# Optimization experiments

Hardware: AMD Instinct MI355X
Metric: run time of the kernel (lower is better)

## Reference

```python
import jax, jax.numpy as jnp
import numpy as np

N_WIRES = 8
DIM = 1 << N_WIRES  # 256

# Precompute CNOT permutations (torchquantum convention: wire 0 = MSB)
_idx = np.arange(DIM)
_CNOT_PERMS = []
for _c in range(N_WIRES):
    _t = (_c + 1) % N_WIRES
    _cbit = (_idx >> (N_WIRES - 1 - _c)) & 1
    _CNOT_PERMS.append(np.where(_cbit == 1, _idx ^ (1 << (N_WIRES - 1 - _t)), _idx))
# PauliZ signs per wire: [DIM, N_WIRES]
_ZSIGNS = np.stack([1.0 - 2.0 * ((_idx >> (N_WIRES - 1 - w)) & 1) for w in range(N_WIRES)], axis=1).astype(np.float32)


def _quantum_heads(x, theta):
    """x: [B,S,H,8] angles; theta: [8]. Returns PauliZ expectations [B,S,H,8].

    Simulates per (token,head) an 8-qubit circuit: RX(x_i+theta_i) on wire i
    (encoder RX followed by trainable RX on same wire = one RX with summed angle),
    then CNOT ring 0->1..6->7, 7->0, then MeasureAll PauliZ.
    """
    B, S, H, _ = x.shape
    N = B * S * H
    ang = x.reshape(N, N_WIRES) + theta  # [N,8]
    state = jnp.zeros((N, DIM), dtype=jnp.complex64).at[:, 0].set(1.0)
    half = ang * 0.5
    c_all = jnp.cos(half)
    s_all = jnp.sin(half)
    for w in range(N_WIRES):
        A = 1 << w
        Bdim = 1 << (N_WIRES - 1 - w)
        s = state.reshape(N, A, 2, Bdim)
        a0, a1 = s[:, :, 0, :], s[:, :, 1, :]
        c = c_all[:, w][:, None, None].astype(jnp.complex64)
        isn = (1j * s_all[:, w][:, None, None]).astype(jnp.complex64)
        n0 = c * a0 - isn * a1
        n1 = -isn * a0 + c * a1
        state = jnp.stack([n0, n1], axis=2).reshape(N, DIM)
    for perm in _CNOT_PERMS:
        state = state[:, perm]
    probs = state.real ** 2 + state.imag ** 2  # [N,256]
    exp = probs @ jnp.asarray(_ZSIGNS)  # [N,8]
    return exp.reshape(B, S, H, N_WIRES)


def _mha(proj, W_combine, num_heads):
    # proj: [B,S,E]; q = k = v = proj (identical deterministic projections)
    B, S, E = proj.shape
    d_k = E // num_heads
    qkv = proj.reshape(B, S, num_heads, d_k).transpose(0, 2, 1, 3)  # [B,H,S,dk]
    scores = jnp.einsum('bhqd,bhkd->bhqk', qkv, qkv) / jnp.sqrt(jnp.float32(d_k))
    attn = jax.nn.softmax(scores, axis=-1)
    out = jnp.einsum('bhqk,bhkd->bhqd', attn, qkv)
    out = out.transpose(0, 2, 1, 3).reshape(B, S, E)
    return out @ W_combine.T


def setup_inputs() -> dict:
    key = jax.random.key(0)
    k1, k2, k3 = jax.random.split(key, 3)
    B, S, H = 8, 1024, 8
    E = H * N_WIRES  # 64
    x = jax.random.normal(k1, (B, S, E), dtype=jnp.float32)
    theta = jax.random.normal(k2, (N_WIRES,), dtype=jnp.float32)
    W_combine = jax.random.normal(k3, (E, E), dtype=jnp.float32) * (1.0 / np.sqrt(E))
    return {'x': x, 'theta': theta, 'W_combine': W_combine}


def reference(x, theta, W_combine):
    B, S, E = x.shape
    H = E // N_WIRES
    proj = _quantum_heads(x.reshape(B, S, H, N_WIRES), theta).reshape(B, S, E)
    return _mha(proj, W_combine, H)
```

## Files before the change

### kernel.cpp

```cpp
#include <hip/hip_runtime.h>

typedef _Float16 half4v __attribute__((ext_vector_type(4)));
typedef __fp16 fp16x2 __attribute__((ext_vector_type(2)));
typedef float float4v __attribute__((ext_vector_type(4)));

#define S_ 1024
#define H_ 8
#define B_ 8
#define BH 64
#define NROW 8192
#define E_ 64
#define VST 1032

static __device__ inline half4v pack4(float a, float b, float c, float d) {
    union { fp16x2 f2[2]; half4v h4; } u;
    u.f2[0] = __builtin_amdgcn_cvt_pkrtz(a, b);
    u.f2[1] = __builtin_amdgcn_cvt_pkrtz(c, d);
    return u.h4;
}

static __device__ inline half4v pack4rne(float a, float b, float c, float d) {
    half4v r = {(_Float16)a, (_Float16)b, (_Float16)c, (_Float16)d};
    return r;
}

__global__ __launch_bounds__(256, 4) void attn_kernel(
        const float* __restrict__ x, const float* __restrict__ theta,
        _Float16* __restrict__ attnH) {
    __shared__ _Float16 kF[64 * 128];
    __shared__ _Float16 vT[9 * VST];
    int bh = blockIdx.x;
    int b = bh >> 3, h = bh & 7;
    int tid = threadIdx.x;

    float th[8];
#pragma unroll
    for (int i = 0; i < 8; ++i) th[i] = theta[i];

    {
        const half4v one = {(_Float16)1.f, (_Float16)1.f, (_Float16)1.f, (_Float16)1.f};
        *(half4v*)&vT[8 * VST + tid * 4] = one;
    }

    for (int s = tid; s < S_; s += 256) {
        const float4* xp = (const float4*)(x + (((size_t)(b << 10) + s) << 6) + (h << 3));
        float4 x0 = xp[0];
        float4 x1 = xp[1];
        float c0 = __cosf(x0.x + th[0]);
        float c1 = __cosf(x0.y + th[1]);
        float c2 = __cosf(x0.z + th[2]);
        float c3 = __cosf(x0.w + th[3]);
        float c4 = __cosf(x1.x + th[4]);
        float c5 = __cosf(x1.y + th[5]);
        float c6 = __cosf(x1.z + th[6]);
        float c7 = __cosf(x1.w + th[7]);
        float e1 = c0 * c1;
        float e2 = e1 * c2;
        float e3 = e2 * c3;
        float e4 = e3 * c4;
        float e5 = e4 * c5;
        float e6 = e5 * c6;
        float e7 = e6 * c7;
        float e0 = ((c1 * c2) * (c3 * c4)) * ((c5 * c6) * c7);
        half4v lo = pack4(e0, e1, e2, e3);
        half4v hi = pack4(e4, e5, e6, e7);
        int kt = s >> 4, c = s & 15;
        *(half4v*)&kF[kt * 128 + c * 4]      = lo;
        *(half4v*)&kF[kt * 128 + 64 + c * 4] = hi;
        vT[0 * VST + s] = lo[0]; vT[1 * VST + s] = lo[1];
        vT[2 * VST + s] = lo[2]; vT[3 * VST + s] = lo[3];
        vT[4 * VST + s] = hi[0]; vT[5 * VST + s] = hi[1];
        vT[6 * VST + s] = hi[2]; vT[7 * VST + s] = hi[3];
    }
    __syncthreads();

    int lane = tid & 63;
    int wv   = tid >> 6;
    int col  = lane & 15;
    int quad = lane >> 4;
    int q0   = blockIdx.y * 64 + wv * 16;

    bool lo2 = (quad < 2);

    int kbase = (lane & 31) * 4;
    int vcol = (col < 9) ? col : (col - 8);
    int vbase = vcol * VST + quad * 4;

    half4v qf = {(_Float16)0.f, (_Float16)0.f, (_Float16)0.f, (_Float16)0.f};
    if (lo2) qf = *(const half4v*)&kF[kbase + (q0 >> 4) * 128];
    qf *= (_Float16)0.51012921f;

    const float4v zc = {0.f, 0.f, 0.f, 0.f};
    float4v o0 = zc, o1 = zc, o2 = zc, o3 = zc;

#pragma unroll
    for (int kt = 0; kt < 16; ++kt) {
        half4v k0 = *(const half4v*)&kF[kbase + (kt +  0) * 128];
        half4v k1 = *(const half4v*)&kF[kbase + (kt + 16) * 128];
        half4v k2 = *(const half4v*)&kF[kbase + (kt + 32) * 128];
        half4v k3 = *(const half4v*)&kF[kbase + (kt + 48) * 128];
        half4v v0 = *(const half4v*)&vT[vbase + (kt +  0) * 16];
        half4v v1 = *(const half4v*)&vT[vbase + (kt + 16) * 16];
        half4v v2 = *(const half4v*)&vT[vbase + (kt + 32) * 16];
        half4v v3 = *(const half4v*)&vT[vbase + (kt + 48) * 16];
        float4v s0 = __builtin_amdgcn_mfma_f32_16x16x16f16(k0, qf, zc, 0, 0, 0);
        float4v s1 = __builtin_amdgcn_mfma_f32_16x16x16f16(k1, qf, zc, 0, 0, 0);
        float4v s2 = __builtin_amdgcn_mfma_f32_16x16x16f16(k2, qf, zc, 0, 0, 0);
        float4v s3 = __builtin_amdgcn_mfma_f32_16x16x16f16(k3, qf, zc, 0, 0, 0);
        half4v p0 = pack4(__builtin_amdgcn_exp2f(s0[0]), __builtin_amdgcn_exp2f(s0[1]),
                          __builtin_amdgcn_exp2f(s0[2]), __builtin_amdgcn_exp2f(s0[3]));
        half4v p1 = pack4(__builtin_amdgcn_exp2f(s1[0]), __builtin_amdgcn_exp2f(s1[1]),
                          __builtin_amdgcn_exp2f(s1[2]), __builtin_amdgcn_exp2f(s1[3]));
        half4v p2 = pack4(__builtin_amdgcn_exp2f(s2[0]), __builtin_amdgcn_exp2f(s2[1]),
                          __builtin_amdgcn_exp2f(s2[2]), __builtin_amdgcn_exp2f(s2[3]));
        half4v p3 = pack4(__builtin_amdgcn_exp2f(s3[0]), __builtin_amdgcn_exp2f(s3[1]),
                          __builtin_amdgcn_exp2f(s3[2]), __builtin_amdgcn_exp2f(s3[3]));
        o0 = __builtin_amdgcn_mfma_f32_16x16x16f16(v0, p0, o0, 0, 0, 0);
        o1 = __builtin_amdgcn_mfma_f32_16x16x16f16(v1, p1, o1, 0, 0, 0);
        o2 = __builtin_amdgcn_mfma_f32_16x16x16f16(v2, p2, o2, 0, 0, 0);
        o3 = __builtin_amdgcn_mfma_f32_16x16x16f16(v3, p3, o3, 0, 0, 0);
    }

    float4v oacc;
#pragma unroll
    for (int r = 0; r < 4; ++r) oacc[r] = (o0[r] + o1[r]) + (o2[r] + o3[r]);

    float l = __shfl(oacc[0], 32 | col, 64);
    if (lo2) {
        float inv = __builtin_amdgcn_rcpf(l);
        half4v ov = pack4(oacc[0] * inv, oacc[1] * inv, oacc[2] * inv, oacc[3] * inv);
        *(half4v*)(attnH + (((size_t)(b << 10) + q0 + col) << 6) + (h << 3) + quad * 4) = ov;
    }
}

__global__ __launch_bounds__(64) void combine_kernel(
        const _Float16* __restrict__ AH, const float* __restrict__ W,
        float* __restrict__ out) {
    int r0 = blockIdx.x * 16;
    int lane = threadIdx.x;
    int col = lane & 15;
    int quad = lane >> 4;

    half4v af[4];
#pragma unroll
    for (int t = 0; t < 4; ++t)
        af[t] = *(const half4v*)&AH[(size_t)(r0 + col) * 64 + t * 16 + quad * 4];

    float4v acc[4] = {{0,0,0,0},{0,0,0,0},{0,0,0,0},{0,0,0,0}};
#pragma unroll
    for (int e = 0; e < 4; ++e) {
#pragma unroll
        for (int t = 0; t < 4; ++t) {
            float4 w4 = *(const float4*)&W[(size_t)(e * 16 + col) * 64 + t * 16 + quad * 4];
            half4v wf = pack4rne(w4.x, w4.y, w4.z, w4.w);
            acc[e] = __builtin_amdgcn_mfma_f32_16x16x16f16(af[t], wf, acc[e], 0, 0, 0);
        }
    }

#pragma unroll
    for (int e = 0; e < 4; ++e)
#pragma unroll
        for (int r = 0; r < 4; ++r)
            out[(size_t)(r0 + quad * 4 + r) * E_ + e * 16 + col] = acc[e][r];
}

extern "C" void kernel_launch(void* const* d_in, const int* in_sizes, int n_in,
                              void* d_out, int out_size, void* d_ws, size_t ws_size,
                              hipStream_t stream) {
    const float* x     = (const float*)d_in[0];
    const float* theta = (const float*)d_in[1];
    const float* W     = (const float*)d_in[2];
    float* out = (float*)d_out;

    _Float16* attnH = (_Float16*)d_ws;

    attn_kernel<<<dim3(BH, S_ / 64), 256, 0, stream>>>(x, theta, attnH);
    combine_kernel<<<NROW / 16, 64, 0, stream>>>(attnH, W, out);
}
```

Measured before the change: 72.44 us.

## Split quantum projection into separate kernel and stage K/V from global

The per-head quantum expectation computation, previously redone by each of the 16 query-tile blocks per (b,h), moves into a dedicated proj_kernel that writes fp16 K and transposed V layouts to workspace once. The attention kernel then bulk-copies these precomputed tiles into LDS with 16-byte loads. This removes 16x redundant cosine and product work per head, at the cost of an extra kernel launch and a global round-trip for K/V. The RNE weight pack helper is also inlined.

```diff
diff --git a/kernel.cpp b/kernel.cpp
--- a/kernel.cpp
+++ b/kernel.cpp
@@ -11,6 +11,8 @@
 #define NROW 8192
 #define E_ 64
 #define VST 1032
+#define VHALVES (9 * VST)
+#define VCHUNK (VHALVES / 8)
 
 static __device__ inline half4v pack4(float a, float b, float c, float d) {
     union { fp16x2 f2[2]; half4v h4; } u;
@@ -19,58 +21,69 @@
     return u.h4;
 }
 
-static __device__ inline half4v pack4rne(float a, float b, float c, float d) {
-    half4v r = {(_Float16)a, (_Float16)b, (_Float16)c, (_Float16)d};
-    return r;
+__global__ __launch_bounds__(256) void proj_kernel(
+        const float* __restrict__ x, const float* __restrict__ theta,
+        _Float16* __restrict__ kG, _Float16* __restrict__ vG) {
+    int bh = blockIdx.x >> 2;
+    int s  = ((blockIdx.x & 3) << 8) + threadIdx.x;
+    int b = bh >> 3, h = bh & 7;
+
+    const float4* xp = (const float4*)(x + (((size_t)(b << 10) + s) << 6) + (h << 3));
+    float4 x0 = xp[0];
+    float4 x1 = xp[1];
+    float c0 = __cosf(x0.x + theta[0]);
+    float c1 = __cosf(x0.y + theta[1]);
+    float c2 = __cosf(x0.z + theta[2]);
+    float c3 = __cosf(x0.w + theta[3]);
+    float c4 = __cosf(x1.x + theta[4]);
+    float c5 = __cosf(x1.y + theta[5]);
+    float c6 = __cosf(x1.z + theta[6]);
+    float c7 = __cosf(x1.w + theta[7]);
+    float e1 = c0 * c1;
+    float e2 = e1 * c2;
+    float e3 = e2 * c3;
+    float e4 = e3 * c4;
+    float e5 = e4 * c5;
+    float e6 = e5 * c6;
+    float e7 = e6 * c7;
+    float e0 = ((c1 * c2) * (c3 * c4)) * ((c5 * c6) * c7);
+    half4v lo = pack4(e0, e1, e2, e3);
+    half4v hi = pack4(e4, e5, e6, e7);
+
+    _Float16* kgb = kG + (size_t)bh * 8192;
+    _Float16* vgb = vG + (size_t)bh * VHALVES;
+    int kt = s >> 4, c = s & 15;
+    *(half4v*)&kgb[kt * 128 + c * 4]      = lo;
+    *(half4v*)&kgb[kt * 128 + 64 + c * 4] = hi;
+    vgb[0 * VST + s] = lo[0]; vgb[1 * VST + s] = lo[1];
+    vgb[2 * VST + s] = lo[2]; vgb[3 * VST + s] = lo[3];
+    vgb[4 * VST + s] = hi[0]; vgb[5 * VST + s] = hi[1];
+    vgb[6 * VST + s] = hi[2]; vgb[7 * VST + s] = hi[3];
+    if ((blockIdx.x & 3) == 0) {
+        const half4v one = {(_Float16)1.f, (_Float16)1.f, (_Float16)1.f, (_Float16)1.f};
+        *(half4v*)&vgb[8 * VST + threadIdx.x * 4] = one;
+    }
 }
 
 __global__ __launch_bounds__(256, 4) void attn_kernel(
-        const float* __restrict__ x, const float* __restrict__ theta,
+        const _Float16* __restrict__ kG, const _Float16* __restrict__ vG,
         _Float16* __restrict__ attnH) {
     __shared__ _Float16 kF[64 * 128];
-    __shared__ _Float16 vT[9 * VST];
+    __shared__ _Float16 vT[VHALVES];
     int bh = blockIdx.x;
     int b = bh >> 3, h = bh & 7;
     int tid = threadIdx.x;
 
-    float th[8];
+    {
+        const uint4* kg4 = (const uint4*)(kG + (size_t)bh * 8192);
+        uint4* kf4 = (uint4*)kF;
 #pragma unroll
-    for (int i = 0; i < 8; ++i) th[i] = theta[i];
-
-    {
-        const half4v one = {(_Float16)1.f, (_Float16)1.f, (_Float16)1.f, (_Float16)1.f};
-        *(half4v*)&vT[8 * VST + tid * 4] = one;
-    }
-
-    for (int s = tid; s < S_; s += 256) {
-        const float4* xp = (const float4*)(x + (((size_t)(b << 10) + s) << 6) + (h << 3));
-        float4 x0 = xp[0];
-        float4 x1 = xp[1];
-        float c0 = __cosf(x0.x + th[0]);
-        float c1 = __cosf(x0.y + th[1]);
-        float c2 = __cosf(x0.z + th[2]);
-        float c3 = __cosf(x0.w + th[3]);
-        float c4 = __cosf(x1.x + th[4]);
-        float c5 = __cosf(x1.y + th[5]);
-        float c6 = __cosf(x1.z + th[6]);
-        float c7 = __cosf(x1.w + th[7]);
-        float e1 = c0 * c1;
-        float e2 = e1 * c2;
-        float e3 = e2 * c3;
-        float e4 = e3 * c4;
-        float e5 = e4 * c5;
-        float e6 = e5 * c6;
-        float e7 = e6 * c7;
-        float e0 = ((c1 * c2) * (c3 * c4)) * ((c5 * c6) * c7);
-        half4v lo = pack4(e0, e1, e2, e3);
-        half4v hi = pack4(e4, e5, e6, e7);
-        int kt = s >> 4, c = s & 15;
-        *(half4v*)&kF[kt * 128 + c * 4]      = lo;
-        *(half4v*)&kF[kt * 128 + 64 + c * 4] = hi;
-        vT[0 * VST + s] = lo[0]; vT[1 * VST + s] = lo[1];
-        vT[2 * VST + s] = lo[2]; vT[3 * VST + s] = lo[3];
-        vT[4 * VST + s] = hi[0]; vT[5 * VST + s] = hi[1];
-        vT[6 * VST + s] = hi[2]; vT[7 * VST + s] = hi[3];
+        for (int i = 0; i < 4; ++i) kf4[tid + i * 256] = kg4[tid + i * 256];
+        const uint4* vg4 = (const uint4*)(vG + (size_t)bh * VHALVES);
+        uint4* vt4 = (uint4*)vT;
+#pragma unroll
+        for (int i = 0; i < 4; ++i) vt4[tid + i * 256] = vg4[tid + i * 256];
+        if (tid < VCHUNK - 1024) vt4[tid + 1024] = vg4[tid + 1024];
     }
     __syncthreads();
 
@@ -152,7 +165,7 @@
 #pragma unroll
         for (int t = 0; t < 4; ++t) {
             float4 w4 = *(const float4*)&W[(size_t)(e * 16 + col) * 64 + t * 16 + quad * 4];
-            half4v wf = pack4rne(w4.x, w4.y, w4.z, w4.w);
+            half4v wf = {(_Float16)w4.x, (_Float16)w4.y, (_Float16)w4.z, (_Float16)w4.w};
             acc[e] = __builtin_amdgcn_mfma_f32_16x16x16f16(af[t], wf, acc[e], 0, 0, 0);
         }
     }
@@ -172,8 +185,11 @@
     const float* W     = (const float*)d_in[2];
     float* out = (float*)d_out;
 
-    _Float16* attnH = (_Float16*)d_ws;
+    _Float16* kG    = (_Float16*)d_ws;
+    _Float16* vG    = (_Float16*)((char*)d_ws + (2 << 20));
+    _Float16* attnH = (_Float16*)((char*)d_ws + (4 << 20));
 
-    attn_kernel<<<dim3(BH, S_ / 64), 256, 0, stream>>>(x, theta, attnH);
+    proj_kernel<<<BH * 4, 256, 0, stream>>>(x, theta, kG, vG);
+    attn_kernel<<<dim3(BH, S_ / 64), 256, 0, stream>>>(kG, vG, attnH);
     combine_kernel<<<NROW / 16, 64, 0, stream>>>(attnH, W, out);
 }
```

Result: no change. 72.31 us (-0.2%).
